# Performance work log

Measured on AMD Instinct MI355X. Metric: run time of the kernel, lower is better.

The kernel has to match this reference:

```python
import jax, jax.numpy as jnp
import numpy as np

DIM = 1024
HEADS = 16
EPS = 1e-5  # torch nn.LayerNorm default
SCALE = (DIM / HEADS) ** -0.5


def _layernorm(x, w, b):
    mu = jnp.mean(x, axis=-1, keepdims=True)
    var = jnp.mean((x - mu) ** 2, axis=-1, keepdims=True)
    return (x - mu) * jax.lax.rsqrt(var + EPS) * w + b


def setup_inputs() -> dict:
    key = jax.random.key(0)
    ks = jax.random.split(key, 12)
    B, Lq, Lk, C, g = 2, 1024, 2048, DIM, HEADS
    c = C // g
    inp = {
        "q": jax.random.normal(ks[0], (B, Lq, C), jnp.float32),
        "k": jax.random.normal(ks[1], (B, Lk, C), jnp.float32),
        "v": jax.random.normal(ks[2], (B, Lk, C), jnp.float32),
        "qpos": jax.random.normal(ks[3], (B, Lq, g, c), jnp.float32),
        "kpos": jax.random.normal(ks[4], (B, Lk, g, c), jnp.float32),
        "mask": jax.random.randint(ks[5], (B, 1, 1, Lk), 0, 2, jnp.int32),
        # LayerNorm params
        "ln_q_w": jnp.ones((C,), jnp.float32),
        "ln_q_b": jnp.zeros((C,), jnp.float32),
        "ln_k_w": jnp.ones((C,), jnp.float32),
        "ln_k_b": jnp.zeros((C,), jnp.float32),
        "ln_v_w": jnp.ones((C,), jnp.float32),
        "ln_v_b": jnp.zeros((C,), jnp.float32),
        # Linear weights, torch layout [out, in]; qkv_bias=False
        "w_q": jax.random.normal(ks[6], (C, C), jnp.float32) * 0.02,
        "w_k": jax.random.normal(ks[7], (C, C), jnp.float32) * 0.02,
        "w_v": jax.random.normal(ks[8], (C, C), jnp.float32) * 0.02,
        "w_proj": jax.random.normal(ks[9], (C, C), jnp.float32) * 0.02,
        "b_proj": jnp.zeros((C,), jnp.float32),
    }
    return inp


def reference(q, k, v, qpos, kpos, mask,
              ln_q_w, ln_q_b, ln_k_w, ln_k_b, ln_v_w, ln_v_b,
              w_q, w_k, w_v, w_proj, b_proj):
    B, Lq, C = q.shape
    g = HEADS
    c = C // g
    Lk = k.shape[1]

    # apply_pos: pos is [B, N, g, c]; add per-head then flatten back
    q = (q.reshape(B, Lq, g, c) + qpos).reshape(B, Lq, C)
    k = (k.reshape(B, Lk, g, c) + kpos).reshape(B, Lk, C)

    qn = _layernorm(q, ln_q_w, ln_q_b)
    kn = _layernorm(k, ln_k_w, ln_k_b)
    vn = _layernorm(v, ln_v_w, ln_v_b)

    # torch Linear: x @ W.T
    q4 = jnp.einsum('bnc,dc->bnd', qn, w_q).reshape(B, Lq, g, c)
    k4 = jnp.einsum('bnc,dc->bnd', kn, w_k).reshape(B, Lk, g, c)
    v4 = jnp.einsum('bnc,dc->bnd', vn, w_v).reshape(B, Lk, g, c)

    # scores: [B, q, g, k] (note head dim is axis 2, matching original einsum)
    attn = jnp.einsum('bqgc,bkgc->bqgk', q4, k4) * SCALE
    m = mask.astype(bool)  # [B,1,1,Lk] broadcasts over q and g
    attn = jnp.where(m, -jnp.inf, attn)
    p = jax.nn.softmax(attn, axis=-1)
    p = jnp.where(m, 0.0, p)

    out = jnp.einsum('bqgk,bkgc->bqgc', p, v4).reshape(B, Lq, C)
    out = jnp.einsum('bnc,dc->bnd', out, w_proj) + b_proj
    return out
```

## Files before the change

### kernel.cpp

```cpp
#include <hip/hip_runtime.h>
#include <stdint.h>
#include <stddef.h>

typedef __bf16 bf16;
typedef bf16 bf16x2 __attribute__((ext_vector_type(2)));
typedef bf16 bf16x4 __attribute__((ext_vector_type(4)));
typedef bf16 bf16x8 __attribute__((ext_vector_type(8)));
typedef float f32x4 __attribute__((ext_vector_type(4)));
typedef float f32x16 __attribute__((ext_vector_type(16)));

#define MFMA16(a, b, c) __builtin_amdgcn_mfma_f32_16x16x32_bf16((a), (b), (c), 0, 0, 0)
#define MFMA32(a, b, c) __builtin_amdgcn_mfma_f32_32x32x16_bf16((a), (b), (c), 0, 0, 0)

#define GLD_LDS16(g, l)                                          \
    __builtin_amdgcn_global_load_lds(                            \
        (const __attribute__((address_space(1))) void*)(g),      \
        (__attribute__((address_space(3))) void*)(l), 16, 0, 0)

__global__ __launch_bounds__(256) void prep_all(const float* __restrict__ wq,
                                                const float* __restrict__ wk,
                                                const float* __restrict__ wv,
                                                const float* __restrict__ wp,
                                                bf16* __restrict__ wout,
                                                const float* __restrict__ q,
                                                const float* __restrict__ k,
                                                const float* __restrict__ v,
                                                const float* __restrict__ qpos,
                                                const float* __restrict__ kpos,
                                                const float* __restrict__ lnqw,
                                                const float* __restrict__ lnqb,
                                                const float* __restrict__ lnkw,
                                                const float* __restrict__ lnkb,
                                                const float* __restrict__ lnvw,
                                                const float* __restrict__ lnvb,
                                                bf16* __restrict__ out) {
    int bx = blockIdx.x;
    int t = threadIdx.x;
    if (bx < 4096) {
        int i = (bx * 256 + t) * 4;
        const float* src;
        int j = i;
        if (i < (1 << 20)) { src = wq; }
        else if (i < (2 << 20)) { src = wk; j = i - (1 << 20); }
        else if (i < (3 << 20)) { src = wv; j = i - (2 << 20); }
        else { src = wp; j = i - (3 << 20); }
        float4 vv = *(const float4*)(src + j);
        bf16x4 o;
        o[0] = (bf16)vv.x; o[1] = (bf16)vv.y; o[2] = (bf16)vv.z; o[3] = (bf16)vv.w;
        *(bf16x4*)(wout + i) = o;
        return;
    }
    int row = bx - 4096;
    const float *x, *pos, *w, *bb;
    int r = row;
    if (row < 2048)      { x = q; pos = qpos; w = lnqw; bb = lnqb; }
    else if (row < 6144) { r = row - 2048; x = k; pos = kpos; w = lnkw; bb = lnkb; }
    else                 { r = row - 6144; x = v; pos = nullptr; w = lnvw; bb = lnvb; }

    float4 vv = ((const float4*)(x + (size_t)r * 1024))[t];
    if (pos != nullptr) {
        float4 p = ((const float4*)(pos + (size_t)r * 1024))[t];
        vv.x += p.x; vv.y += p.y; vv.z += p.z; vv.w += p.w;
    }
    float s1 = vv.x + vv.y + vv.z + vv.w;
    float s2 = vv.x * vv.x + vv.y * vv.y + vv.z * vv.z + vv.w * vv.w;
#pragma unroll
    for (int off = 1; off < 64; off <<= 1) {
        s1 += __shfl_xor(s1, off);
        s2 += __shfl_xor(s2, off);
    }
    __shared__ float red[8];
    int wave = t >> 6;
    if ((t & 63) == 0) { red[wave * 2] = s1; red[wave * 2 + 1] = s2; }
    __syncthreads();
    s1 = red[0] + red[2] + red[4] + red[6];
    s2 = red[1] + red[3] + red[5] + red[7];
    float mu = s1 * (1.0f / 1024.0f);
    float var = s2 * (1.0f / 1024.0f) - mu * mu;
    float rstd = rsqrtf(var + 1e-5f);
    float4 wv4 = ((const float4*)w)[t];
    float4 bv4 = ((const float4*)bb)[t];
    bf16x4 o;
    o[0] = (bf16)((vv.x - mu) * rstd * wv4.x + bv4.x);
    o[1] = (bf16)((vv.y - mu) * rstd * wv4.y + bv4.y);
    o[2] = (bf16)((vv.z - mu) * rstd * wv4.z + bv4.z);
    o[3] = (bf16)((vv.w - mu) * rstd * wv4.w + bv4.w);
    *(bf16x4*)(out + (size_t)row * 1024 + t * 4) = o;
}

__global__ __launch_bounds__(256) void gemm_qkv(const bf16* __restrict__ A,
                                                const bf16* __restrict__ w0,
                                                const bf16* __restrict__ w1,
                                                const bf16* __restrict__ w2,
                                                bf16* __restrict__ out,
                                                bf16* __restrict__ vt) {
    __shared__ bf16 As[2][128 * 32];
    __shared__ bf16 Bs[2][128 * 32];
    int bxr = blockIdx.x;
    int bx = (bxr & 7) * 80 + (bxr >> 3);
    int tileN = bx & 7;
    int tileM = bx >> 3;
    int t = threadIdx.x;
    int wave = t >> 6, lane = t & 63;
    int lr = lane & 15, lg = lane >> 4;
    int wr = wave >> 1, wc = wave & 1;
    int co = (lg ^ ((lr >> 1) & 3)) << 4;
    int rowBase = tileM * 128;
    const bf16* W = (rowBase < 2048) ? w0 : ((rowBase < 6144) ? w1 : w2);
    const bf16* Ab = A + (size_t)rowBase * 1024;
    const bf16* Wb = W + (size_t)(tileN * 128) * 1024;

    int o0 = t, o1 = t + 256;
    int sr0 = o0 >> 2, sc0 = (o0 & 3) ^ ((sr0 >> 1) & 3);
    int sr1 = o1 >> 2, sc1 = (o1 & 3) ^ ((sr1 >> 1) & 3);

#define QSTAGE(bufi, k0n)                                                     \
    {                                                                         \
        GLD_LDS16(Ab + (size_t)sr0 * 1024 + (k0n) + sc0 * 8,                  \
                  (char*)As[bufi] + o0 * 16);                                 \
        GLD_LDS16(Ab + (size_t)sr1 * 1024 + (k0n) + sc1 * 8,                  \
                  (char*)As[bufi] + o1 * 16);                                 \
        GLD_LDS16(Wb + (size_t)sr0 * 1024 + (k0n) + sc0 * 8,                  \
                  (char*)Bs[bufi] + o0 * 16);                                 \
        GLD_LDS16(Wb + (size_t)sr1 * 1024 + (k0n) + sc1 * 8,                  \
                  (char*)Bs[bufi] + o1 * 16);                                 \
    }

    const f32x4 zero4 = {0.f, 0.f, 0.f, 0.f};
    f32x4 acc[4][4];
#pragma unroll
    for (int i = 0; i < 4; ++i)
#pragma unroll
        for (int j = 0; j < 4; ++j) acc[i][j] = zero4;

    QSTAGE(0, 0);
    __syncthreads();
    int gbuf = 0;
    for (int k0 = 0; k0 < 1024; k0 += 32) {
        __builtin_amdgcn_s_barrier();
        if (k0 + 32 < 1024) {
            QSTAGE(gbuf ^ 1, k0 + 32);
            asm volatile("s_waitcnt vmcnt(4)" ::: "memory");
        } else {
            asm volatile("s_waitcnt vmcnt(0)" ::: "memory");
        }
        __builtin_amdgcn_s_barrier();
        bf16x8 af[4], bfr[4];
#pragma unroll
        for (int mf = 0; mf < 4; ++mf)
            af[mf] = *(const bf16x8*)((const char*)As[gbuf] +
                                      (wr * 64 + mf * 16 + lr) * 64 + co);
#pragma unroll
        for (int nf = 0; nf < 4; ++nf)
            bfr[nf] = *(const bf16x8*)((const char*)Bs[gbuf] +
                                       (wc * 64 + nf * 16 + lr) * 64 + co);
        __builtin_amdgcn_s_setprio(1);
#pragma unroll
        for (int mf = 0; mf < 4; ++mf)
#pragma unroll
            for (int nf = 0; nf < 4; ++nf)
                acc[mf][nf] = MFMA16(af[mf], bfr[nf], acc[mf][nf]);
        __builtin_amdgcn_s_setprio(0);
        gbuf ^= 1;
    }
#undef QSTAGE
    bool isV = (rowBase >= 6144);
    if (!isV) {
#pragma unroll
        for (int nf = 0; nf < 4; ++nf) {
            int ncol = tileN * 128 + wc * 64 + nf * 16 + lr;
#pragma unroll
            for (int mf = 0; mf < 4; ++mf) {
                int mrow = rowBase + wr * 64 + mf * 16 + lg * 4;
#pragma unroll
                for (int r = 0; r < 4; ++r)
                    out[(size_t)(mrow + r) * 1024 + ncol] = (bf16)acc[mf][nf][r];
            }
        }
    } else {
        int b2 = (rowBase - 6144) >> 11;
        int kb = rowBase - 6144 - (b2 << 11);
#pragma unroll
        for (int nf = 0; nf < 4; ++nf) {
            int ncol = tileN * 128 + wc * 64 + nf * 16 + lr;
            int h2 = ncol >> 6, d2 = ncol & 63;
            bf16* vrow = vt + ((size_t)((b2 * 16 + h2) * 64 + d2)) * 2048;
#pragma unroll
            for (int mf = 0; mf < 4; ++mf) {
                int kk = kb + wr * 64 + mf * 16 + lg * 4;
                bf16x4 pv;
#pragma unroll
                for (int r = 0; r < 4; ++r) pv[r] = (bf16)acc[mf][nf][r];
                *(bf16x4*)(vrow + kk) = pv;
            }
        }
    }
}

__global__ __launch_bounds__(256) void gemm_proj(const bf16* __restrict__ A,
                                                 const bf16* __restrict__ w0,
                                                 const float* __restrict__ bias,
                                                 float* __restrict__ out) {
    __shared__ bf16 As[2][64 * 32];
    __shared__ bf16 Bs[2][128 * 32];
    int bxr = blockIdx.x;
    int bx = (bxr & 7) * 32 + (bxr >> 3);
    int tileN = bx & 7;
    int tileM = bx >> 3;
    int t = threadIdx.x;
    int wave = t >> 6, lane = t & 63;
    int lr = lane & 15, lg = lane >> 4;
    int wc = wave;
    int rowBase = tileM * 64;
    const bf16* Ab = A + (size_t)rowBase * 1024;
    const bf16* Wb = w0 + (size_t)(tileN * 128) * 1024;

    int o16b0 = wave * 128 + lane;
    int o16b1 = o16b0 + 64;

#define PSTAGE(bufi, k0n)                                                     \
    {                                                                         \
        GLD_LDS16(Ab + (size_t)(t >> 2) * 1024 + (k0n) + (t & 3) * 8,         \
                  (char*)As[bufi] + t * 16);                                  \
        GLD_LDS16(Wb + (size_t)(o16b0 >> 2) * 1024 + (k0n) + (o16b0 & 3) * 8, \
                  (char*)Bs[bufi] + o16b0 * 16);                              \
        GLD_LDS16(Wb + (size_t)(o16b1 >> 2) * 1024 + (k0n) + (o16b1 & 3) * 8, \
                  (char*)Bs[bufi] + o16b1 * 16);                              \
    }

    const f32x4 zero4 = {0.f, 0.f, 0.f, 0.f};
    f32x4 acc[4][2];
#pragma unroll
    for (int i = 0; i < 4; ++i) { acc[i][0] = zero4; acc[i][1] = zero4; }

    PSTAGE(0, 0);
    __syncthreads();
    int gbuf = 0;
    for (int k0 = 0; k0 < 1024; k0 += 32) {
        __builtin_amdgcn_s_barrier();
        if (k0 + 32 < 1024) {
            PSTAGE(gbuf ^ 1, k0 + 32);
            asm volatile("s_waitcnt vmcnt(3)" ::: "memory");
        } else {
            asm volatile("s_waitcnt vmcnt(0)" ::: "memory");
        }
        __builtin_amdgcn_s_barrier();
        bf16x8 af[4], bfr[2];
#pragma unroll
        for (int mf = 0; mf < 4; ++mf)
            af[mf] = *(const bf16x8*)((const char*)As[gbuf] +
                                      (mf * 16 + lr) * 64 + lg * 16);
#pragma unroll
        for (int nf = 0; nf < 2; ++nf)
            bfr[nf] = *(const bf16x8*)((const char*)Bs[gbuf] +
                                       (wc * 32 + nf * 16 + lr) * 64 + lg * 16);
        __builtin_amdgcn_s_setprio(1);
#pragma unroll
        for (int mf = 0; mf < 4; ++mf)
#pragma unroll
            for (int nf = 0; nf < 2; ++nf)
                acc[mf][nf] = MFMA16(af[mf], bfr[nf], acc[mf][nf]);
        __builtin_amdgcn_s_setprio(0);
        gbuf ^= 1;
    }
#undef PSTAGE
#pragma unroll
    for (int nf = 0; nf < 2; ++nf) {
        int ncol = tileN * 128 + wc * 32 + nf * 16 + lr;
        float bv = bias[ncol];
#pragma unroll
        for (int mf = 0; mf < 4; ++mf) {
            int mrow = rowBase + mf * 16 + lg * 4;
#pragma unroll
            for (int r = 0; r < 4; ++r)
                out[(size_t)(mrow + r) * 1024 + ncol] = acc[mf][nf][r] + bv;
        }
    }
}

__global__ __launch_bounds__(256, 3) void attn_kernel(const bf16* __restrict__ qkv4,
                                                      const bf16* __restrict__ vt,
                                                      const int* __restrict__ mask,
                                                      bf16* __restrict__ opart,
                                                      float* __restrict__ ml) {
    __shared__ float bias_s[512];
    __shared__ bf16 Ks[3][64 * 64];
    __shared__ bf16 Vs[3][64 * 64];
    int bx = blockIdx.x;
    bx = (bx & 7) * 128 + (bx >> 3);
    int split = bx & 3, qt = (bx >> 2) & 7, h = (bx >> 5) & 15, b = bx >> 9;
    int t = threadIdx.x;
    int wave = t >> 6, lane = t & 63, lq = lane & 31, hi = lane >> 5;
    int lq7 = lq & 7;

    const float SHIFT = 30.0f;
    const int* mrow = mask + b * 2048 + split * 512;
    for (int i = t; i < 512; i += 256) bias_s[i] = mrow[i] ? -1e30f : -SHIFT;

    int qbase = qt * 128 + wave * 32;
    const bf16* qptr = qkv4 + ((size_t)(b * 1024 + qbase + lq)) * 1024 + h * 64 + hi * 8;
    bf16x8 qf[4];
#pragma unroll
    for (int s = 0; s < 4; ++s) qf[s] = *(const bf16x8*)(qptr + s * 16);

    const bf16* kpanel = qkv4 + (size_t)(2048 + b * 2048 + split * 512) * 1024 + h * 64;
    const bf16* vpanel = vt + ((size_t)((b * 16 + h) * 64)) * 2048 + split * 512;

    int r0 = t >> 3, c0 = (t & 7) ^ (r0 & 7);
    int r1 = r0 + 32, c1 = (t & 7) ^ (r1 & 7);

#define STAGE(bufi, lkn)                                                      \
    {                                                                         \
        GLD_LDS16(kpanel + (size_t)((lkn) + r0) * 1024 + c0 * 8,              \
                  (char*)Ks[bufi] + t * 16);                                  \
        GLD_LDS16(kpanel + (size_t)((lkn) + r1) * 1024 + c1 * 8,              \
                  (char*)Ks[bufi] + (t + 256) * 16);                          \
        GLD_LDS16(vpanel + (size_t)r0 * 2048 + (lkn) + c0 * 8,                \
                  (char*)Vs[bufi] + t * 16);                                  \
        GLD_LDS16(vpanel + (size_t)r1 * 2048 + (lkn) + c1 * 8,                \
                  (char*)Vs[bufi] + (t + 256) * 16);                          \
    }

    f32x16 accO0 = {}, accO1 = {};
    float l_run = 0.0f;
    const float C_QK = 0.18033688011112042f;

#define PROCESS(bufi, s2, kloc)                                               \
    {                                                                         \
        const char* kb_ = (const char*)Ks[bufi] + ((s2) * 32 + lq) * 128;     \
        bf16x8 kf0 = *(const bf16x8*)(kb_ + (((hi + 0) ^ lq7) << 4));         \
        bf16x8 kf1 = *(const bf16x8*)(kb_ + (((hi + 2) ^ lq7) << 4));         \
        bf16x8 kf2 = *(const bf16x8*)(kb_ + (((hi + 4) ^ lq7) << 4));         \
        bf16x8 kf3 = *(const bf16x8*)(kb_ + (((hi + 6) ^ lq7) << 4));         \
        f32x16 S = {};                                                        \
        __builtin_amdgcn_s_setprio(1);                                        \
        S = MFMA32(kf0, qf[0], S);                                            \
        S = MFMA32(kf1, qf[1], S);                                            \
        S = MFMA32(kf2, qf[2], S);                                            \
        S = MFMA32(kf3, qf[3], S);                                            \
        __builtin_amdgcn_s_setprio(0);                                        \
        f32x4 bv0 = *(const f32x4*)&bias_s[(kloc) + 4 * hi];                  \
        f32x4 bv1 = *(const f32x4*)&bias_s[(kloc) + 8 + 4 * hi];              \
        f32x4 bv2 = *(const f32x4*)&bias_s[(kloc) + 16 + 4 * hi];             \
        f32x4 bv3 = *(const f32x4*)&bias_s[(kloc) + 24 + 4 * hi];             \
        float p[16];                                                          \
        _Pragma("unroll")                                                     \
        for (int r = 0; r < 16; ++r) {                                        \
            float bvr = (r < 4 ? bv0[r & 3] : r < 8 ? bv1[r & 3]              \
                         : r < 12 ? bv2[r & 3] : bv3[r & 3]);                 \
            p[r] = __builtin_amdgcn_exp2f(fmaf(S[r], C_QK, bvr));             \
        }                                                                     \
        l_run += ((p[0] + p[1]) + (p[2] + p[3])) + ((p[4] + p[5]) + (p[6] + p[7])) \
               + ((p[8] + p[9]) + (p[10] + p[11])) + ((p[12] + p[13]) + (p[14] + p[15])); \
        union { unsigned u[4]; bf16x8 v; } pf0, pf1;                          \
        _Pragma("unroll")                                                     \
        for (int w = 0; w < 4; ++w) {                                         \
            union { bf16x2 h2; unsigned u; } cv;                              \
            cv.h2[0] = (bf16)p[2 * w]; cv.h2[1] = (bf16)p[2 * w + 1];         \
            pf0.u[w] = cv.u;                                                  \
            cv.h2[0] = (bf16)p[8 + 2 * w]; cv.h2[1] = (bf16)p[9 + 2 * w];     \
            pf1.u[w] = cv.u;                                                  \
        }                                                                     \
        const char* vbA = (const char*)Vs[bufi] + lq * 128 + hi * 8;          \
        const char* vbB = vbA + 32 * 128;                                     \
        bf16x4 va[8];                                                         \
        _Pragma("unroll")                                                     \
        for (int m = 0; m < 4; ++m) {                                         \
            int cofs = ((((s2) * 4 + m) ^ lq7) << 4);                         \
            va[m] = *(const bf16x4*)(vbA + cofs);                             \
            va[4 + m] = *(const bf16x4*)(vbB + cofs);                         \
        }                                                                     \
        bf16x8 va0 = __builtin_shufflevector(va[0], va[1], 0, 1, 2, 3, 4, 5, 6, 7); \
        bf16x8 va1 = __builtin_shufflevector(va[2], va[3], 0, 1, 2, 3, 4, 5, 6, 7); \
        bf16x8 va2 = __builtin_shufflevector(va[4], va[5], 0, 1, 2, 3, 4, 5, 6, 7); \
        bf16x8 va3 = __builtin_shufflevector(va[6], va[7], 0, 1, 2, 3, 4, 5, 6, 7); \
        __builtin_amdgcn_s_setprio(1);                                        \
        accO0 = MFMA32(va0, pf0.v, accO0);                                    \
        accO0 = MFMA32(va1, pf1.v, accO0);                                    \
        accO1 = MFMA32(va2, pf0.v, accO1);                                    \
        accO1 = MFMA32(va3, pf1.v, accO1);                                    \
        __builtin_amdgcn_s_setprio(0);                                        \
    }

    STAGE(0, 0);
    __syncthreads();
    STAGE(1, 64);
#pragma unroll
    for (int it = 0; it < 8; ++it) {
        __builtin_amdgcn_s_barrier();
        if (it + 2 < 8) {
            STAGE((it + 2) % 3, (it + 2) * 64);
            asm volatile("s_waitcnt vmcnt(8)" ::: "memory");
        } else if (it == 6) {
            asm volatile("s_waitcnt vmcnt(4)" ::: "memory");
        } else {
            asm volatile("s_waitcnt vmcnt(0)" ::: "memory");
        }
        __builtin_amdgcn_s_barrier();
        PROCESS(it % 3, 0, it * 64);
        PROCESS(it % 3, 1, it * 64 + 32);
    }
#undef STAGE
#undef PROCESS

    l_run += __shfl_xor(l_run, 32);

    float linv = (l_run > 0.0f) ? (1.0f / l_run) : 0.0f;
    size_t orow = (size_t)(split * 2048 + b * 1024 + qbase + lq);
    bf16* op = opart + orow * 1024 + h * 64;
#pragma unroll
    for (int m = 0; m < 4; ++m) {
        bf16x4 y0, y1;
#pragma unroll
        for (int r = 0; r < 4; ++r) {
            y0[r] = (bf16)(accO0[4 * m + r] * linv);
            y1[r] = (bf16)(accO1[4 * m + r] * linv);
        }
        *(bf16x4*)(op + 8 * m + 4 * hi) = y0;
        *(bf16x4*)(op + 32 + 8 * m + 4 * hi) = y1;
    }
    if (lane < 32) {
        float2 mlv = {SHIFT, l_run};
        *(float2*)(ml + (orow * 16 + h) * 2) = mlv;
    }
}

__global__ __launch_bounds__(256) void combine_kernel(const bf16* __restrict__ opart,
                                                      const float* __restrict__ ml,
                                                      bf16* __restrict__ out) {
    int row = blockIdx.x;
    int t = threadIdx.x;
    int h = t >> 4;
    float m[4], l[4];
#pragma unroll
    for (int s = 0; s < 4; ++s) {
        const float* p = ml + ((size_t)(s * 2048 + row) * 16 + h) * 2;
        m[s] = p[0]; l[s] = p[1];
    }
    float M = fmaxf(fmaxf(m[0], m[1]), fmaxf(m[2], m[3]));
    float u[4], denom = 0.0f;
#pragma unroll
    for (int s = 0; s < 4; ++s) { u[s] = exp2f(m[s] - M) * l[s]; denom += u[s]; }
    float inv = (denom > 0.0f) ? (1.0f / denom) : 0.0f;
    float acc[4] = {0.f, 0.f, 0.f, 0.f};
#pragma unroll
    for (int s = 0; s < 4; ++s) {
        bf16x4 y = *(const bf16x4*)(opart + (size_t)(s * 2048 + row) * 1024 + t * 4);
#pragma unroll
        for (int c = 0; c < 4; ++c) acc[c] += u[s] * (float)y[c];
    }
    bf16x4 r;
#pragma unroll
    for (int c = 0; c < 4; ++c) r[c] = (bf16)(acc[c] * inv);
    *(bf16x4*)(out + (size_t)row * 1024 + t * 4) = r;
}

extern "C" void kernel_launch(void* const* d_in, const int* in_sizes, int n_in,
                              void* d_out, int out_size, void* d_ws, size_t ws_size,
                              hipStream_t stream) {
    const float* q    = (const float*)d_in[0];
    const float* k    = (const float*)d_in[1];
    const float* v    = (const float*)d_in[2];
    const float* qpos = (const float*)d_in[3];
    const float* kpos = (const float*)d_in[4];
    const int*   mask = (const int*)d_in[5];
    const float* lnqw = (const float*)d_in[6];
    const float* lnqb = (const float*)d_in[7];
    const float* lnkw = (const float*)d_in[8];
    const float* lnkb = (const float*)d_in[9];
    const float* lnvw = (const float*)d_in[10];
    const float* lnvb = (const float*)d_in[11];
    const float* wq   = (const float*)d_in[12];
    const float* wk   = (const float*)d_in[13];
    const float* wv   = (const float*)d_in[14];
    const float* wp   = (const float*)d_in[15];
    const float* bp   = (const float*)d_in[16];
    float* out = (float*)d_out;

    char* ws = (char*)d_ws;
    const size_t MB = 1024 * 1024;
    bf16*  w_all = (bf16*)(ws + 0 * MB);
    bf16*  wq_b  = (bf16*)(ws + 0 * MB);
    bf16*  wk_b  = (bf16*)(ws + 2 * MB);
    bf16*  wv_b  = (bf16*)(ws + 4 * MB);
    bf16*  wp_b  = (bf16*)(ws + 6 * MB);
    bf16*  xn    = (bf16*)(ws + 8 * MB);
    bf16*  opart = (bf16*)(ws + 8 * MB);
    float* mlbuf = (float*)(ws + 24 * MB);
    bf16*  qkv4  = (bf16*)(ws + 28 * MB);
    bf16*  vtb   = (bf16*)(ws + 40 * MB);
    bf16*  attn  = (bf16*)(ws + 0 * MB);

    prep_all<<<14336, 256, 0, stream>>>(wq, wk, wv, wp, w_all,
                                        q, k, v, qpos, kpos,
                                        lnqw, lnqb, lnkw, lnkb, lnvw, lnvb, xn);

    gemm_qkv<<<640, 256, 0, stream>>>(xn, wq_b, wk_b, wv_b, qkv4, vtb);

    attn_kernel<<<1024, 256, 0, stream>>>(qkv4, vtb, mask, opart, mlbuf);

    combine_kernel<<<2048, 256, 0, stream>>>(opart, mlbuf, attn);

    gemm_proj<<<256, 256, 0, stream>>>(attn, wp_b, bp, out);
}
```

Measured before the change: 108.4 us.

## Fuse split-KV combine into projection GEMM A-operand staging

Removes the separate combine kernel. The projection GEMM now computes per-row, per-head combine weights from the stored max/sum values into LDS, loads the four split-KV partial outputs into registers and stores their weighted sum as the bf16 A tile. This saves a kernel launch and the write and re-read of the combined attention buffer. In exchange, each of the 8 N-tile blocks per M-tile redoes the combine and reads four times the A data, and the A path moves from async direct-to-LDS loads to register loads plus VALU work, with more complex waitcnt bookkeeping.

```diff
diff --git a/kernel.cpp b/kernel.cpp
--- a/kernel.cpp
+++ b/kernel.cpp
@@ -197,12 +197,14 @@
     }
 }
 
-__global__ __launch_bounds__(256) void gemm_proj(const bf16* __restrict__ A,
-                                                 const bf16* __restrict__ w0,
-                                                 const float* __restrict__ bias,
-                                                 float* __restrict__ out) {
+__global__ __launch_bounds__(256) void gemm_proj_fused(const bf16* __restrict__ opart,
+                                                       const float* __restrict__ ml,
+                                                       const bf16* __restrict__ w0,
+                                                       const float* __restrict__ bias,
+                                                       float* __restrict__ out) {
     __shared__ bf16 As[2][64 * 32];
     __shared__ bf16 Bs[2][128 * 32];
+    __shared__ f32x4 wlds[64][17];
     int bxr = blockIdx.x;
     int bx = (bxr & 7) * 32 + (bxr >> 3);
     int tileN = bx & 7;
@@ -212,16 +214,54 @@
     int lr = lane & 15, lg = lane >> 4;
     int wc = wave;
     int rowBase = tileM * 64;
-    const bf16* Ab = A + (size_t)rowBase * 1024;
     const bf16* Wb = w0 + (size_t)(tileN * 128) * 1024;
+
+    for (int p = t; p < 1024; p += 256) {
+        int row = p >> 4, h = p & 15;
+        float m[4], l[4];
+#pragma unroll
+        for (int s = 0; s < 4; ++s) {
+            const float* mp = ml + ((size_t)(s * 2048 + rowBase + row) * 16 + h) * 2;
+            m[s] = mp[0]; l[s] = mp[1];
+        }
+        float M = fmaxf(fmaxf(m[0], m[1]), fmaxf(m[2], m[3]));
+        float u[4], den = 0.0f;
+#pragma unroll
+        for (int s = 0; s < 4; ++s) { u[s] = exp2f(m[s] - M) * l[s]; den += u[s]; }
+        float inv = (den > 0.0f) ? (1.0f / den) : 0.0f;
+        f32x4 w4 = {u[0] * inv, u[1] * inv, u[2] * inv, u[3] * inv};
+        wlds[row][h] = w4;
+    }
+
+    int arow = t >> 2, ac8 = (t & 3) * 8;
+    const bf16* apart = opart + (size_t)(rowBase + arow) * 1024 + ac8;
+    bf16x8 ar0, ar1, ar2, ar3;
+
+#define ALOAD(k0n)                                                            \
+    {                                                                         \
+        ar0 = *(const bf16x8*)(apart + (size_t)0 * 2097152 + (k0n));          \
+        ar1 = *(const bf16x8*)(apart + (size_t)1 * 2097152 + (k0n));          \
+        ar2 = *(const bf16x8*)(apart + (size_t)2 * 2097152 + (k0n));          \
+        ar3 = *(const bf16x8*)(apart + (size_t)3 * 2097152 + (k0n));          \
+    }
+
+#define ACOMBINE(bufi, k0n)                                                   \
+    {                                                                         \
+        f32x4 w4 = wlds[arow][(k0n) >> 6];                                    \
+        bf16x8 cv;                                                            \
+        _Pragma("unroll")                                                     \
+        for (int j = 0; j < 8; ++j) {                                         \
+            float a = w4[0] * (float)ar0[j] + w4[1] * (float)ar1[j]           \
+                    + w4[2] * (float)ar2[j] + w4[3] * (float)ar3[j];          \
+            cv[j] = (bf16)a;                                                  \
+        }                                                                     \
+        *(bf16x8*)((char*)As[bufi] + t * 16) = cv;                            \
+    }
 
     int o16b0 = wave * 128 + lane;
     int o16b1 = o16b0 + 64;
-
-#define PSTAGE(bufi, k0n)                                                     \
+#define BSTAGE(bufi, k0n)                                                     \
     {                                                                         \
-        GLD_LDS16(Ab + (size_t)(t >> 2) * 1024 + (k0n) + (t & 3) * 8,         \
-                  (char*)As[bufi] + t * 16);                                  \
         GLD_LDS16(Wb + (size_t)(o16b0 >> 2) * 1024 + (k0n) + (o16b0 & 3) * 8, \
                   (char*)Bs[bufi] + o16b0 * 16);                              \
         GLD_LDS16(Wb + (size_t)(o16b1 >> 2) * 1024 + (k0n) + (o16b1 & 3) * 8, \
@@ -233,16 +273,29 @@
 #pragma unroll
     for (int i = 0; i < 4; ++i) { acc[i][0] = zero4; acc[i][1] = zero4; }
 
-    PSTAGE(0, 0);
+    ALOAD(0);
     __syncthreads();
+    ACOMBINE(0, 0);
+    BSTAGE(0, 0);
+    ALOAD(32);
+    __syncthreads();
+
     int gbuf = 0;
-    for (int k0 = 0; k0 < 1024; k0 += 32) {
+    for (int it = 0; it < 32; ++it) {
+        int k0 = it * 32;
         __builtin_amdgcn_s_barrier();
-        if (k0 + 32 < 1024) {
-            PSTAGE(gbuf ^ 1, k0 + 32);
-            asm volatile("s_waitcnt vmcnt(3)" ::: "memory");
+        if (it + 1 < 32) {
+            ACOMBINE(gbuf ^ 1, k0 + 32);
+            if (it + 2 < 32) ALOAD(k0 + 64);
+            BSTAGE(gbuf ^ 1, k0 + 32);
+            if (it + 2 < 32) {
+                asm volatile("s_waitcnt vmcnt(6)" ::: "memory");
+            } else {
+                asm volatile("s_waitcnt vmcnt(2)" ::: "memory");
+            }
+            asm volatile("s_waitcnt lgkmcnt(0)" ::: "memory");
         } else {
-            asm volatile("s_waitcnt vmcnt(0)" ::: "memory");
+            asm volatile("s_waitcnt vmcnt(0) lgkmcnt(0)" ::: "memory");
         }
         __builtin_amdgcn_s_barrier();
         bf16x8 af[4], bfr[2];
@@ -263,7 +316,9 @@
         __builtin_amdgcn_s_setprio(0);
         gbuf ^= 1;
     }
-#undef PSTAGE
+#undef ALOAD
+#undef ACOMBINE
+#undef BSTAGE
 #pragma unroll
     for (int nf = 0; nf < 2; ++nf) {
         int ncol = tileN * 128 + wc * 32 + nf * 16 + lr;
@@ -425,36 +480,6 @@
     }
 }
 
-__global__ __launch_bounds__(256) void combine_kernel(const bf16* __restrict__ opart,
-                                                      const float* __restrict__ ml,
-                                                      bf16* __restrict__ out) {
-    int row = blockIdx.x;
-    int t = threadIdx.x;
-    int h = t >> 4;
-    float m[4], l[4];
-#pragma unroll
-    for (int s = 0; s < 4; ++s) {
-        const float* p = ml + ((size_t)(s * 2048 + row) * 16 + h) * 2;
-        m[s] = p[0]; l[s] = p[1];
-    }
-    float M = fmaxf(fmaxf(m[0], m[1]), fmaxf(m[2], m[3]));
-    float u[4], denom = 0.0f;
-#pragma unroll
-    for (int s = 0; s < 4; ++s) { u[s] = exp2f(m[s] - M) * l[s]; denom += u[s]; }
-    float inv = (denom > 0.0f) ? (1.0f / denom) : 0.0f;
-    float acc[4] = {0.f, 0.f, 0.f, 0.f};
-#pragma unroll
-    for (int s = 0; s < 4; ++s) {
-        bf16x4 y = *(const bf16x4*)(opart + (size_t)(s * 2048 + row) * 1024 + t * 4);
-#pragma unroll
-        for (int c = 0; c < 4; ++c) acc[c] += u[s] * (float)y[c];
-    }
-    bf16x4 r;
-#pragma unroll
-    for (int c = 0; c < 4; ++c) r[c] = (bf16)(acc[c] * inv);
-    *(bf16x4*)(out + (size_t)row * 1024 + t * 4) = r;
-}
-
 extern "C" void kernel_launch(void* const* d_in, const int* in_sizes, int n_in,
                               void* d_out, int out_size, void* d_ws, size_t ws_size,
                               hipStream_t stream) {
@@ -489,7 +514,6 @@
     float* mlbuf = (float*)(ws + 24 * MB);
     bf16*  qkv4  = (bf16*)(ws + 28 * MB);
     bf16*  vtb   = (bf16*)(ws + 40 * MB);
-    bf16*  attn  = (bf16*)(ws + 0 * MB);
 
     prep_all<<<14336, 256, 0, stream>>>(wq, wk, wv, wp, w_all,
                                         q, k, v, qpos, kpos,
@@ -499,7 +523,5 @@
 
     attn_kernel<<<1024, 256, 0, stream>>>(qkv4, vtb, mask, opart, mlbuf);
 
-    combine_kernel<<<2048, 256, 0, stream>>>(opart, mlbuf, attn);
-
-    gemm_proj<<<256, 256, 0, stream>>>(attn, wp_b, bp, out);
+    gemm_proj_fused<<<256, 256, 0, stream>>>(opart, mlbuf, wp_b, bp, out);
 }
```

Result: slower. 117.3 us (+8.2%).
